# Kernel tuning notes

Hardware: AMD Instinct MI355X
Metric: run time of the kernel (lower is better)

## Reference

```python
import jax, jax.numpy as jnp
import numpy as np

N_NODES = 50000
N_EDGES = 400000
IN_DIM = 64
HID = 128
HEADS = 4
NEG_SLOPE = 0.2


def gat_conv(x, src, dst, W, a_src, a_dst, b, heads, out_ch, concat):
    N = x.shape[0]
    h = (x @ W).reshape(N, heads, out_ch)                 # [N,H,C]
    alpha_s = jnp.einsum('nhc,hc->nh', h, a_src)          # [N,H]
    alpha_d = jnp.einsum('nhc,hc->nh', h, a_dst)
    e = jax.nn.leaky_relu(alpha_s[src] + alpha_d[dst], NEG_SLOPE)  # [E,H]
    m = jax.ops.segment_max(e, dst, num_segments=N)
    m = jnp.where(jnp.isfinite(m), m, 0.0)
    ex = jnp.exp(e - m[dst])
    s = jax.ops.segment_sum(ex, dst, num_segments=N)
    alpha = ex / s[dst]                                   # segment softmax over incoming edges
    out = jax.ops.segment_sum(h[src] * alpha[:, :, None], dst, num_segments=N)  # [N,H,C]
    out = out.reshape(N, heads * out_ch) if concat else out.mean(axis=1)
    return out + b


def setup_inputs() -> dict:
    key = jax.random.key(0)
    ks = jax.random.split(key, 20)
    g = lambda i, shape, sc: (jax.random.normal(ks[i], shape, jnp.float32) * sc)
    x = g(0, (N_NODES, IN_DIM), 1.0)
    edge_index = jax.random.randint(ks[1], (2, N_EDGES), 0, N_NODES, dtype=jnp.int32)
    d = {
        'x': x, 'edge_index': edge_index,
        'W1': g(2, (IN_DIM, HEADS * HID), 0.1), 'a_src1': g(3, (HEADS, HID), 0.1), 'a_dst1': g(4, (HEADS, HID), 0.1), 'b1': jnp.zeros((HEADS * HID,), jnp.float32),
        'W2': g(5, (HEADS * HID, HEADS * HID), 0.05), 'a_src2': g(6, (HEADS, HID), 0.1), 'a_dst2': g(7, (HEADS, HID), 0.1), 'b2': jnp.zeros((HEADS * HID,), jnp.float32),
        'W3': g(8, (HEADS * HID, HID), 0.05), 'a_src3': g(9, (1, HID), 0.1), 'a_dst3': g(10, (1, HID), 0.1), 'b3': jnp.zeros((HID,), jnp.float32),
        'fc1_w': g(11, (HID, HID // 2), 0.1), 'fc1_b': jnp.zeros((HID // 2,), jnp.float32),
        'fc2_w': g(12, (HID // 2, 1), 0.1), 'fc2_b': jnp.zeros((1,), jnp.float32),
    }
    return d


def reference(x, edge_index, W1, a_src1, a_dst1, b1, W2, a_src2, a_dst2, b2, W3, a_src3, a_dst3, b3, fc1_w, fc1_b, fc2_w, fc2_b):
    N = x.shape[0]
    loop = jnp.arange(N, dtype=edge_index.dtype)
    src = jnp.concatenate([edge_index[0], loop])  # PyG GATConv adds self-loops by default
    dst = jnp.concatenate([edge_index[1], loop])
    h = jax.nn.elu(gat_conv(x, src, dst, W1, a_src1, a_dst1, b1, HEADS, HID, True))
    h = jax.nn.elu(gat_conv(h, src, dst, W2, a_src2, a_dst2, b2, HEADS, HID, True))
    h = jax.nn.elu(gat_conv(h, src, dst, W3, a_src3, a_dst3, b3, 1, HID, False))
    h = jax.nn.relu(h @ fc1_w + fc1_b)
    return jax.nn.sigmoid(h @ fc2_w + fc2_b)  # [N, 1]
```

## Files before the change

### kernel.cpp

```cpp
#include <hip/hip_runtime.h>
#include <math.h>

typedef __attribute__((ext_vector_type(8))) short short8;
typedef __attribute__((ext_vector_type(4))) float f32x4;
typedef unsigned short u16;
typedef unsigned int u32;

__device__ inline u16 f2b(float f) {
  u32 u = __float_as_uint(f);
  return (u16)((u + 0x7FFFu + ((u >> 16) & 1u)) >> 16);
}
__device__ inline float b2f(u16 b) { return __uint_as_float((u32)b << 16); }
__device__ inline float lrelu(float v) { return v > 0.f ? v : 0.2f * v; }

__device__ inline void gld_lds16(const void* g, void* l) {
  __builtin_amdgcn_global_load_lds((const __attribute__((address_space(1))) void*)g,
                                   (__attribute__((address_space(3))) void*)l, 16, 0, 0);
}

__global__ void cast_f32_bf16(const float* __restrict__ src, u16* __restrict__ dst, int n) {
  int i = blockIdx.x * blockDim.x + threadIdx.x;
  if (i < n) dst[i] = f2b(src[i]);
}

__global__ void cast_transpose_w(const float* __restrict__ W, u16* __restrict__ Wt, int K,
                                 int HC) {
  int i = blockIdx.x * blockDim.x + threadIdx.x;
  if (i >= K * HC) return;
  int k = i / HC, n = i % HC;
  Wt[(size_t)n * K + k] = f2b(W[i]);
}

__global__ __launch_bounds__(256) void gemm_bf16_gat(
    const u16* __restrict__ A, const u16* __restrict__ Bt, u16* __restrict__ Hb,
    const float* __restrict__ a_src, const float* __restrict__ a_dst,
    float* __restrict__ aS, float* __restrict__ aD, int M, int HC, int K, int Hh) {
  __shared__ u16 As[128 * 32];
  __shared__ u16 Bs[128 * 32];
  __shared__ float sRed[2][2][128];
  const int tid = threadIdx.x;
  const int w = tid >> 6, lane = tid & 63;
  const int wm = w >> 1, wn = w & 1;
  const int q = lane >> 4, l15 = lane & 15;
  const int nBase = blockIdx.x * 128;
  const int mBase = blockIdx.y * 128;
  const int h = nBase >> 7;
  const int srow = lane >> 2;
  const int skc = (lane & 3) * 8;

  f32x4 acc[4][4];
#pragma unroll
  for (int i = 0; i < 4; ++i)
#pragma unroll
    for (int j = 0; j < 4; ++j) acc[i][j] = (f32x4){0.f, 0.f, 0.f, 0.f};

  for (int k0 = 0; k0 < K; k0 += 32) {
#pragma unroll
    for (int r = 0; r < 2; ++r) {
      int lrow = w * 32 + r * 16 + srow;
      int ga = mBase + lrow;
      if (ga >= M) ga = M - 1;
      gld_lds16(A + (size_t)ga * K + k0 + skc, &As[(w * 32 + r * 16) * 32]);
      int gb = nBase + lrow;
      gld_lds16(Bt + (size_t)gb * K + k0 + skc, &Bs[(w * 32 + r * 16) * 32]);
    }
    __syncthreads();
    short8 af[4], bf[4];
#pragma unroll
    for (int i = 0; i < 4; ++i)
      af[i] = *(const short8*)&As[(wm * 64 + i * 16 + l15) * 32 + q * 8];
#pragma unroll
    for (int j = 0; j < 4; ++j)
      bf[j] = *(const short8*)&Bs[(wn * 64 + j * 16 + l15) * 32 + q * 8];
#pragma unroll
    for (int i = 0; i < 4; ++i)
#pragma unroll
      for (int j = 0; j < 4; ++j)
        acc[i][j] = __builtin_amdgcn_mfma_f32_16x16x32_bf16(af[i], bf[j], acc[i][j], 0, 0, 0);
    __syncthreads();
  }

  float asv[4], adv[4];
#pragma unroll
  for (int j = 0; j < 4; ++j) {
    int cw = wn * 64 + j * 16 + l15;
    asv[j] = a_src[h * 128 + cw];
    adv[j] = a_dst[h * 128 + cw];
  }
#pragma unroll
  for (int mi = 0; mi < 4; ++mi) {
#pragma unroll
    for (int r = 0; r < 4; ++r) {
      int row = mBase + wm * 64 + mi * 16 + q * 4 + r;
      float s = 0.f, d = 0.f;
#pragma unroll
      for (int j = 0; j < 4; ++j) {
        float v = acc[mi][j][r];
        s = fmaf(v, asv[j], s);
        d = fmaf(v, adv[j], d);
        if (row < M) Hb[(size_t)row * HC + nBase + wn * 64 + j * 16 + l15] = f2b(v);
      }
#pragma unroll
      for (int o = 8; o; o >>= 1) {
        s += __shfl_xor(s, o);
        d += __shfl_xor(d, o);
      }
      if (l15 == 0) {
        int lr = wm * 64 + mi * 16 + q * 4 + r;
        sRed[0][wn][lr] = s;
        sRed[1][wn][lr] = d;
      }
    }
  }
  __syncthreads();
  if (tid < 128) {
    int row = mBase + tid;
    if (row < M) {
      aS[(size_t)row * Hh + h] = sRed[0][0][tid] + sRed[0][1][tid];
      aD[(size_t)row * Hh + h] = sRed[1][0][tid] + sRed[1][1][tid];
    }
  }
}

__device__ inline void edge_nodes(const int* __restrict__ ei, int E0, int e, int& s, int& d) {
  if (e < E0) { s = ei[e]; d = ei[E0 + e]; }
  else        { s = e - E0; d = e - E0; }
}

__global__ void deg_count(const int* __restrict__ ei, int E0, int ET, int* __restrict__ deg) {
  int e = blockIdx.x * blockDim.x + threadIdx.x;
  if (e >= ET) return;
  int s, d;
  edge_nodes(ei, E0, e, s, d);
  atomicAdd(&deg[d], 1);
}

__global__ __launch_bounds__(256) void scan_chunk(const int* __restrict__ deg,
                                                  int* __restrict__ incl,
                                                  int* __restrict__ bsums, int N) {
  __shared__ int sdata[256];
  const int t = threadIdx.x;
  const int base = blockIdx.x * 2048;
  int v[8];
  int sum = 0;
#pragma unroll
  for (int i = 0; i < 8; ++i) {
    int idx = base + t * 8 + i;
    v[i] = (idx < N) ? deg[idx] : 0;
    sum += v[i];
  }
  sdata[t] = sum;
  __syncthreads();
  for (int off = 1; off < 256; off <<= 1) {
    int x = (t >= off) ? sdata[t - off] : 0;
    __syncthreads();
    sdata[t] += x;
    __syncthreads();
  }
  int run = (t > 0) ? sdata[t - 1] : 0;
#pragma unroll
  for (int i = 0; i < 8; ++i) {
    int idx = base + t * 8 + i;
    run += v[i];
    if (idx < N) incl[idx] = run;
  }
  if (t == 255) bsums[blockIdx.x] = sdata[255];
}

__global__ __launch_bounds__(256) void scan_bsums(int* __restrict__ bsums, int nb) {
  __shared__ int s[256];
  int t = threadIdx.x;
  s[t] = (t < nb) ? bsums[t] : 0;
  __syncthreads();
  for (int off = 1; off < 256; off <<= 1) {
    int x = (t >= off) ? s[t - off] : 0;
    __syncthreads();
    s[t] += x;
    __syncthreads();
  }
  if (t < nb) bsums[t] = (t == 0) ? 0 : s[t - 1];
}

__global__ void scan_final(const int* __restrict__ incl, const int* __restrict__ bsums,
                           int* __restrict__ rowptr, int N) {
  int i = blockIdx.x * blockDim.x + threadIdx.x;
  if (i < N) rowptr[i + 1] = incl[i] + bsums[i >> 11];
  if (i == 0) rowptr[0] = 0;
}

__global__ void csr_fill(const int* __restrict__ ei, int E0, int ET,
                         const int* __restrict__ rowptr, int* __restrict__ cnt,
                         int* __restrict__ csr_src) {
  int e = blockIdx.x * blockDim.x + threadIdx.x;
  if (e >= ET) return;
  int s, d;
  edge_nodes(ei, E0, e, s, d);
  int pos = atomicAdd(&cnt[d], 1);
  csr_src[rowptr[d] + pos] = s;
}

__global__ __launch_bounds__(256) void gat_fused_agg(
    const int* __restrict__ rowptr, const int* __restrict__ csr_src,
    const u16* __restrict__ Hb, const float* __restrict__ aSb,
    const float* __restrict__ aDb, const float* __restrict__ bias,
    u16* __restrict__ outB, float* __restrict__ outF, int N, int Hh) {
  const int wid = (int)((blockIdx.x * (blockDim.x >> 6)) + (threadIdx.x >> 6));
  const int lane = threadIdx.x & 63;
  if (wid >= N) return;
  const int beg = rowptr[wid];
  const int deg = rowptr[wid + 1] - beg;

  if (Hh == 4) {
    const int h = lane >> 4;
    const int e16 = lane & 15;
    const int c0 = lane * 8;
    const float adh = aDb[(size_t)wid * 4 + h];
    float bv[8];
    *(float4*)&bv[0] = *(const float4*)&bias[c0];
    *(float4*)&bv[4] = *(const float4*)&bias[c0 + 4];
    float m = -1e30f, ssum = 0.f;
    float acc[8] = {};
    for (int c = 0; c < deg; c += 16) {
      const int ce = min(16, deg - c);
      int srcv = 0;
      float l = -1e30f;
      if (e16 < ce) {
        srcv = csr_src[beg + c + e16];
        l = lrelu(aSb[(size_t)srcv * 4 + h] + adh);
      }
      float cm = l;
#pragma unroll
      for (int o = 8; o; o >>= 1) cm = fmaxf(cm, __shfl_xor(cm, o));
      float newm = fmaxf(m, cm);
      float r = expf(m - newm);
      m = newm;
      float pexp = expf(l - m);
      float cs = pexp;
#pragma unroll
      for (int o = 8; o; o >>= 1) cs += __shfl_xor(cs, o);
      ssum = ssum * r + cs;
#pragma unroll
      for (int i = 0; i < 8; ++i) acc[i] *= r;
      const int hbase = lane & 48;
      for (int e = 0; e < ce; ++e) {
        int se = __shfl(srcv, e);
        float wgt = __shfl(pexp, hbase | e);
        uint4 pv = *(const uint4*)&Hb[(size_t)se * 512 + c0];
        acc[0] = fmaf(wgt, b2f((u16)(pv.x & 0xffff)), acc[0]);
        acc[1] = fmaf(wgt, b2f((u16)(pv.x >> 16)), acc[1]);
        acc[2] = fmaf(wgt, b2f((u16)(pv.y & 0xffff)), acc[2]);
        acc[3] = fmaf(wgt, b2f((u16)(pv.y >> 16)), acc[3]);
        acc[4] = fmaf(wgt, b2f((u16)(pv.z & 0xffff)), acc[4]);
        acc[5] = fmaf(wgt, b2f((u16)(pv.z >> 16)), acc[5]);
        acc[6] = fmaf(wgt, b2f((u16)(pv.w & 0xffff)), acc[6]);
        acc[7] = fmaf(wgt, b2f((u16)(pv.w >> 16)), acc[7]);
      }
    }
    const float inv = 1.f / ssum;
    u16 packed[8];
#pragma unroll
    for (int i = 0; i < 8; ++i) {
      float v = fmaf(acc[i], inv, bv[i]);
      v = v > 0.f ? v : expm1f(v);
      acc[i] = v;
      packed[i] = f2b(v);
    }
    if (outB) *(uint4*)&outB[(size_t)wid * 512 + c0] = *(const uint4*)packed;
    if (outF) {
      *(float4*)&outF[(size_t)wid * 512 + c0] = make_float4(acc[0], acc[1], acc[2], acc[3]);
      *(float4*)&outF[(size_t)wid * 512 + c0 + 4] =
          make_float4(acc[4], acc[5], acc[6], acc[7]);
    }
  } else {
    const int c0 = lane * 2;
    const float adh = aDb[wid];
    const float bv0 = bias[c0], bv1 = bias[c0 + 1];
    float m = -1e30f, ssum = 0.f;
    float a0 = 0.f, a1 = 0.f;
    for (int c = 0; c < deg; c += 64) {
      const int ce = min(64, deg - c);
      int srcv = 0;
      float l = -1e30f;
      if (lane < ce) {
        srcv = csr_src[beg + c + lane];
        l = lrelu(aSb[srcv] + adh);
      }
      float cm = l;
#pragma unroll
      for (int o = 32; o; o >>= 1) cm = fmaxf(cm, __shfl_xor(cm, o));
      float newm = fmaxf(m, cm);
      float r = expf(m - newm);
      m = newm;
      float pexp = expf(l - m);
      float cs = pexp;
#pragma unroll
      for (int o = 32; o; o >>= 1) cs += __shfl_xor(cs, o);
      ssum = ssum * r + cs;
      a0 *= r;
      a1 *= r;
      for (int e = 0; e < ce; ++e) {
        int se = __shfl(srcv, e);
        float wgt = __shfl(pexp, e);
        u32 pv = *(const u32*)&Hb[(size_t)se * 128 + c0];
        a0 = fmaf(wgt, b2f((u16)(pv & 0xffff)), a0);
        a1 = fmaf(wgt, b2f((u16)(pv >> 16)), a1);
      }
    }
    const float inv = 1.f / ssum;
    float v0 = fmaf(a0, inv, bv0), v1 = fmaf(a1, inv, bv1);
    v0 = v0 > 0.f ? v0 : expm1f(v0);
    v1 = v1 > 0.f ? v1 : expm1f(v1);
    if (outB) {
      u16 pk[2] = {f2b(v0), f2b(v1)};
      *(u32*)&outB[(size_t)wid * 128 + c0] = *(const u32*)pk;
    }
    if (outF) *(float2*)&outF[(size_t)wid * 128 + c0] = make_float2(v0, v1);
  }
}

__global__ __launch_bounds__(256) void fc_head(const float* __restrict__ A,
                                               const float* __restrict__ B,
                                               const float* __restrict__ bias,
                                               const float* __restrict__ w2,
                                               const float* __restrict__ b2,
                                               float* __restrict__ out, int M) {
  __shared__ float As[16][64];
  __shared__ float Bs[16][64];
  __shared__ float sP[64][17];
  const int tid = threadIdx.x;
  const int tx = tid & 15, ty = tid >> 4;
  const int mBase = blockIdx.y * 64;
  const int aRow = tid >> 2;
  const int aK = (tid & 3) << 2;
  const int bC = tid & 63;
  const int bR0 = tid >> 6;
  const int K = 128, N = 64;
  float acc[4][4] = {};
  for (int k0 = 0; k0 < K; k0 += 16) {
    float4 av = make_float4(0.f, 0.f, 0.f, 0.f);
    int gr = mBase + aRow;
    if (gr < M) av = *(const float4*)&A[(size_t)gr * K + k0 + aK];
    As[aK + 0][aRow] = av.x;
    As[aK + 1][aRow] = av.y;
    As[aK + 2][aRow] = av.z;
    As[aK + 3][aRow] = av.w;
#pragma unroll
    for (int i = 0; i < 4; ++i) {
      int r = bR0 + i * 4;
      Bs[r][bC] = B[(size_t)(k0 + r) * N + bC];
    }
    __syncthreads();
#pragma unroll
    for (int k = 0; k < 16; ++k) {
      float4 a = *(const float4*)&As[k][ty * 4];
      float4 b = *(const float4*)&Bs[k][tx * 4];
      float ar[4] = {a.x, a.y, a.z, a.w};
      float br[4] = {b.x, b.y, b.z, b.w};
#pragma unroll
      for (int i = 0; i < 4; ++i)
#pragma unroll
        for (int j = 0; j < 4; ++j) acc[i][j] = fmaf(ar[i], br[j], acc[i][j]);
    }
    __syncthreads();
  }
  float4 bv = *(const float4*)&bias[tx * 4];
  float4 wv = *(const float4*)&w2[tx * 4];
#pragma unroll
  for (int i = 0; i < 4; ++i) {
    float p = 0.f;
    p = fmaf(fmaxf(acc[i][0] + bv.x, 0.f), wv.x, p);
    p = fmaf(fmaxf(acc[i][1] + bv.y, 0.f), wv.y, p);
    p = fmaf(fmaxf(acc[i][2] + bv.z, 0.f), wv.z, p);
    p = fmaf(fmaxf(acc[i][3] + bv.w, 0.f), wv.w, p);
    sP[ty * 4 + i][tx] = p;
  }
  __syncthreads();
  if (tid < 64) {
    int row = mBase + tid;
    if (row < M) {
      float s = 0.f;
#pragma unroll
      for (int t = 0; t < 16; ++t) s += sP[tid][t];
      out[row] = 1.f / (1.f + expf(-(s + b2[0])));
    }
  }
}

extern "C" void kernel_launch(void* const* d_in, const int* in_sizes, int n_in,
                              void* d_out, int out_size, void* d_ws, size_t ws_size,
                              hipStream_t stream) {
  const float* x    = (const float*)d_in[0];
  const int*   ei   = (const int*)d_in[1];
  const float* W1   = (const float*)d_in[2];
  const float* as1  = (const float*)d_in[3];
  const float* ad1  = (const float*)d_in[4];
  const float* b1   = (const float*)d_in[5];
  const float* W2   = (const float*)d_in[6];
  const float* as2  = (const float*)d_in[7];
  const float* ad2  = (const float*)d_in[8];
  const float* b2   = (const float*)d_in[9];
  const float* W3   = (const float*)d_in[10];
  const float* as3  = (const float*)d_in[11];
  const float* ad3  = (const float*)d_in[12];
  const float* b3   = (const float*)d_in[13];
  const float* fc1w = (const float*)d_in[14];
  const float* fc1b = (const float*)d_in[15];
  const float* fc2w = (const float*)d_in[16];
  const float* fc2b = (const float*)d_in[17];
  float* out = (float*)d_out;

  const int N  = in_sizes[0] / 64;
  const int E0 = in_sizes[1] / 2;
  const int ET = E0 + N;

  char* ws = (char*)d_ws;
  size_t off = 0;
  auto alloc = [&](size_t bytes) -> void* {
    void* p = ws + off;
    off += (bytes + 255) & ~(size_t)255;
    return p;
  };
  u16*   bufXb   = (u16*)alloc((size_t)N * 512 * 2);
  u16*   bufHb   = (u16*)alloc((size_t)N * 512 * 2);
  float* bufF    = (float*)alloc((size_t)N * 128 * 4);
  float* aS      = (float*)alloc((size_t)N * 4 * 4);
  float* aD      = (float*)alloc((size_t)N * 4 * 4);
  u16*   Wt1     = (u16*)alloc((size_t)512 * 64 * 2);
  u16*   Wt2     = (u16*)alloc((size_t)512 * 512 * 2);
  u16*   Wt3     = (u16*)alloc((size_t)128 * 512 * 2);
  int*   deg     = (int*)alloc((size_t)N * 4);
  int*   cnt     = (int*)alloc((size_t)N * 4);
  int*   incl    = (int*)alloc((size_t)N * 4);
  int*   rowptr  = (int*)alloc((size_t)(N + 1) * 4);
  int*   bsums   = (int*)alloc(256 * 4);
  int*   csr_src = (int*)alloc((size_t)ET * 4);
  (void)ws_size; (void)n_in; (void)out_size;

  hipLaunchKernelGGL(cast_f32_bf16, dim3((N * 64 + 255) / 256), dim3(256), 0, stream, x,
                     bufXb, N * 64);
  hipLaunchKernelGGL(cast_transpose_w, dim3((64 * 512 + 255) / 256), dim3(256), 0, stream,
                     W1, Wt1, 64, 512);
  hipLaunchKernelGGL(cast_transpose_w, dim3((512 * 512 + 255) / 256), dim3(256), 0, stream,
                     W2, Wt2, 512, 512);
  hipLaunchKernelGGL(cast_transpose_w, dim3((512 * 128 + 255) / 256), dim3(256), 0, stream,
                     W3, Wt3, 512, 128);

  hipMemsetAsync(deg, 0, (size_t)N * 4, stream);
  hipMemsetAsync(cnt, 0, (size_t)N * 4, stream);
  int eb = (ET + 255) / 256;
  hipLaunchKernelGGL(deg_count, dim3(eb), dim3(256), 0, stream, ei, E0, ET, deg);
  int nb = (N + 2047) / 2048;
  hipLaunchKernelGGL(scan_chunk, dim3(nb), dim3(256), 0, stream, deg, incl, bsums, N);
  hipLaunchKernelGGL(scan_bsums, dim3(1), dim3(256), 0, stream, bsums, nb);
  hipLaunchKernelGGL(scan_final, dim3((N + 255) / 256), dim3(256), 0, stream, incl, bsums,
                     rowptr, N);
  hipLaunchKernelGGL(csr_fill, dim3(eb), dim3(256), 0, stream, ei, E0, ET, rowptr, cnt,
                     csr_src);

  const int gy = (N + 127) / 128;
  auto gat_layer = [&](int K, const u16* Wt, const float* a_s, const float* a_d,
                       const float* bias, int Hh, u16* aggB, float* aggF) {
    const int HC = Hh * 128;
    hipLaunchKernelGGL(gemm_bf16_gat, dim3(HC / 128, gy), dim3(256), 0, stream, bufXb, Wt,
                       bufHb, a_s, a_d, aS, aD, N, HC, K, Hh);
    hipLaunchKernelGGL(gat_fused_agg, dim3((N + 3) / 4), dim3(256), 0, stream, rowptr,
                       csr_src, bufHb, aS, aD, bias, aggB, aggF, N, Hh);
  };

  gat_layer(64,  Wt1, as1, ad1, b1, 4, bufXb, nullptr);
  gat_layer(512, Wt2, as2, ad2, b2, 4, bufXb, nullptr);
  gat_layer(512, Wt3, as3, ad3, b3, 1, nullptr, bufF);

  hipLaunchKernelGGL(fc_head, dim3(1, (N + 63) / 64), dim3(256), 0, stream, bufF, fc1w,
                     fc1b, fc2w, fc2b, out, N);
}
```

Before: 475.2 us.

## Fuse prep kernels, drop bsums scan, unroll aggregation gather by four

Merges the x cast, three weight cast-transposes and degree counting into one fused_prep launch, and merges the two memsets into one. The separate bsums scan kernel is removed; scan_final now sums the preceding chunk totals serially per thread. The aggregation loops peel the first chunk to skip the rescale and unroll the edge gather by four so more independent loads are in flight. Together these cut launch overhead and raise memory-level parallelism, at the cost of a branchier prep kernel and redundant bsums reads in scan_final.

```diff
diff --git a/kernel.cpp b/kernel.cpp
--- a/kernel.cpp
+++ b/kernel.cpp
@@ -18,17 +18,40 @@
                                    (__attribute__((address_space(3))) void*)l, 16, 0, 0);
 }
 
-__global__ void cast_f32_bf16(const float* __restrict__ src, u16* __restrict__ dst, int n) {
+__global__ void fused_prep(const float* __restrict__ x, u16* __restrict__ xb, int NX,
+                           const float* __restrict__ W1, u16* __restrict__ Wt1,
+                           const float* __restrict__ W2, u16* __restrict__ Wt2,
+                           const float* __restrict__ W3, u16* __restrict__ Wt3,
+                           const int* __restrict__ ei, int E0, int ET,
+                           int* __restrict__ deg) {
   int i = blockIdx.x * blockDim.x + threadIdx.x;
-  if (i < n) dst[i] = f2b(src[i]);
-}
-
-__global__ void cast_transpose_w(const float* __restrict__ W, u16* __restrict__ Wt, int K,
-                                 int HC) {
-  int i = blockIdx.x * blockDim.x + threadIdx.x;
-  if (i >= K * HC) return;
-  int k = i / HC, n = i % HC;
-  Wt[(size_t)n * K + k] = f2b(W[i]);
+  if (i < NX) {
+    xb[i] = f2b(x[i]);
+    return;
+  }
+  i -= NX;
+  if (i < 64 * 512) {
+    int k = i / 512, n = i % 512;
+    Wt1[n * 64 + k] = f2b(W1[i]);
+    return;
+  }
+  i -= 64 * 512;
+  if (i < 512 * 512) {
+    int k = i / 512, n = i % 512;
+    Wt2[n * 512 + k] = f2b(W2[i]);
+    return;
+  }
+  i -= 512 * 512;
+  if (i < 512 * 128) {
+    int k = i / 128, n = i % 128;
+    Wt3[n * 512 + k] = f2b(W3[i]);
+    return;
+  }
+  i -= 512 * 128;
+  if (i < ET) {
+    int d = (i < E0) ? ei[E0 + i] : (i - E0);
+    atomicAdd(&deg[d], 1);
+  }
 }
 
 __global__ __launch_bounds__(256) void gemm_bf16_gat(
@@ -122,19 +145,6 @@
   }
 }
 
-__device__ inline void edge_nodes(const int* __restrict__ ei, int E0, int e, int& s, int& d) {
-  if (e < E0) { s = ei[e]; d = ei[E0 + e]; }
-  else        { s = e - E0; d = e - E0; }
-}
-
-__global__ void deg_count(const int* __restrict__ ei, int E0, int ET, int* __restrict__ deg) {
-  int e = blockIdx.x * blockDim.x + threadIdx.x;
-  if (e >= ET) return;
-  int s, d;
-  edge_nodes(ei, E0, e, s, d);
-  atomicAdd(&deg[d], 1);
-}
-
 __global__ __launch_bounds__(256) void scan_chunk(const int* __restrict__ deg,
                                                   int* __restrict__ incl,
                                                   int* __restrict__ bsums, int N) {
@@ -167,24 +177,14 @@
   if (t == 255) bsums[blockIdx.x] = sdata[255];
 }
 
-__global__ __launch_bounds__(256) void scan_bsums(int* __restrict__ bsums, int nb) {
-  __shared__ int s[256];
-  int t = threadIdx.x;
-  s[t] = (t < nb) ? bsums[t] : 0;
-  __syncthreads();
-  for (int off = 1; off < 256; off <<= 1) {
-    int x = (t >= off) ? s[t - off] : 0;
-    __syncthreads();
-    s[t] += x;
-    __syncthreads();
-  }
-  if (t < nb) bsums[t] = (t == 0) ? 0 : s[t - 1];
-}
-
 __global__ void scan_final(const int* __restrict__ incl, const int* __restrict__ bsums,
-                           int* __restrict__ rowptr, int N) {
+                           int* __restrict__ rowptr, int N, int nb) {
   int i = blockIdx.x * blockDim.x + threadIdx.x;
-  if (i < N) rowptr[i + 1] = incl[i] + bsums[i >> 11];
+  if (i >= N) return;
+  int chunk = i >> 11;
+  int pre = 0;
+  for (int j = 0; j < chunk; ++j) pre += bsums[j];
+  rowptr[i + 1] = incl[i] + pre;
   if (i == 0) rowptr[0] = 0;
 }
 
@@ -194,7 +194,8 @@
   int e = blockIdx.x * blockDim.x + threadIdx.x;
   if (e >= ET) return;
   int s, d;
-  edge_nodes(ei, E0, e, s, d);
+  if (e < E0) { s = ei[e]; d = ei[E0 + e]; }
+  else        { s = e - E0; d = e - E0; }
   int pos = atomicAdd(&cnt[d], 1);
   csr_src[rowptr[d] + pos] = s;
 }
@@ -214,6 +215,7 @@
     const int h = lane >> 4;
     const int e16 = lane & 15;
     const int c0 = lane * 8;
+    const int hbase = lane & 48;
     const float adh = aDb[(size_t)wid * 4 + h];
     float bv[8];
     *(float4*)&bv[0] = *(const float4*)&bias[c0];
@@ -231,29 +233,55 @@
       float cm = l;
 #pragma unroll
       for (int o = 8; o; o >>= 1) cm = fmaxf(cm, __shfl_xor(cm, o));
-      float newm = fmaxf(m, cm);
-      float r = expf(m - newm);
-      m = newm;
-      float pexp = expf(l - m);
-      float cs = pexp;
-#pragma unroll
-      for (int o = 8; o; o >>= 1) cs += __shfl_xor(cs, o);
-      ssum = ssum * r + cs;
-#pragma unroll
-      for (int i = 0; i < 8; ++i) acc[i] *= r;
-      const int hbase = lane & 48;
-      for (int e = 0; e < ce; ++e) {
+      float pexp, cs;
+      if (c == 0) {
+        m = cm;
+        pexp = expf(l - m);
+        cs = pexp;
+#pragma unroll
+        for (int o = 8; o; o >>= 1) cs += __shfl_xor(cs, o);
+        ssum = cs;
+      } else {
+        float newm = fmaxf(m, cm);
+        float r = expf(m - newm);
+        m = newm;
+        pexp = expf(l - m);
+        cs = pexp;
+#pragma unroll
+        for (int o = 8; o; o >>= 1) cs += __shfl_xor(cs, o);
+        ssum = ssum * r + cs;
+#pragma unroll
+        for (int i = 0; i < 8; ++i) acc[i] *= r;
+      }
+      int e = 0;
+      for (; e + 4 <= ce; e += 4) {
+        int se0 = __shfl(srcv, e + 0), se1 = __shfl(srcv, e + 1);
+        int se2 = __shfl(srcv, e + 2), se3 = __shfl(srcv, e + 3);
+        float w0 = __shfl(pexp, hbase | (e + 0)), w1 = __shfl(pexp, hbase | (e + 1));
+        float w2 = __shfl(pexp, hbase | (e + 2)), w3 = __shfl(pexp, hbase | (e + 3));
+        uint4 p0 = *(const uint4*)&Hb[(size_t)se0 * 512 + c0];
+        uint4 p1 = *(const uint4*)&Hb[(size_t)se1 * 512 + c0];
+        uint4 p2 = *(const uint4*)&Hb[(size_t)se2 * 512 + c0];
+        uint4 p3 = *(const uint4*)&Hb[(size_t)se3 * 512 + c0];
+#define ACC8(pv, wgt)                                             \
+  acc[0] = fmaf(wgt, b2f((u16)(pv.x & 0xffff)), acc[0]);          \
+  acc[1] = fmaf(wgt, b2f((u16)(pv.x >> 16)), acc[1]);             \
+  acc[2] = fmaf(wgt, b2f((u16)(pv.y & 0xffff)), acc[2]);          \
+  acc[3] = fmaf(wgt, b2f((u16)(pv.y >> 16)), acc[3]);             \
+  acc[4] = fmaf(wgt, b2f((u16)(pv.z & 0xffff)), acc[4]);          \
+  acc[5] = fmaf(wgt, b2f((u16)(pv.z >> 16)), acc[5]);             \
+  acc[6] = fmaf(wgt, b2f((u16)(pv.w & 0xffff)), acc[6]);          \
+  acc[7] = fmaf(wgt, b2f((u16)(pv.w >> 16)), acc[7]);
+        ACC8(p0, w0)
+        ACC8(p1, w1)
+        ACC8(p2, w2)
+        ACC8(p3, w3)
+      }
+      for (; e < ce; ++e) {
         int se = __shfl(srcv, e);
         float wgt = __shfl(pexp, hbase | e);
         uint4 pv = *(const uint4*)&Hb[(size_t)se * 512 + c0];
-        acc[0] = fmaf(wgt, b2f((u16)(pv.x & 0xffff)), acc[0]);
-        acc[1] = fmaf(wgt, b2f((u16)(pv.x >> 16)), acc[1]);
-        acc[2] = fmaf(wgt, b2f((u16)(pv.y & 0xffff)), acc[2]);
-        acc[3] = fmaf(wgt, b2f((u16)(pv.y >> 16)), acc[3]);
-        acc[4] = fmaf(wgt, b2f((u16)(pv.z & 0xffff)), acc[4]);
-        acc[5] = fmaf(wgt, b2f((u16)(pv.z >> 16)), acc[5]);
-        acc[6] = fmaf(wgt, b2f((u16)(pv.w & 0xffff)), acc[6]);
-        acc[7] = fmaf(wgt, b2f((u16)(pv.w >> 16)), acc[7]);
+        ACC8(pv, wgt)
       }
     }
     const float inv = 1.f / ssum;
@@ -288,17 +316,46 @@
       float cm = l;
 #pragma unroll
       for (int o = 32; o; o >>= 1) cm = fmaxf(cm, __shfl_xor(cm, o));
-      float newm = fmaxf(m, cm);
-      float r = expf(m - newm);
-      m = newm;
-      float pexp = expf(l - m);
-      float cs = pexp;
-#pragma unroll
-      for (int o = 32; o; o >>= 1) cs += __shfl_xor(cs, o);
-      ssum = ssum * r + cs;
-      a0 *= r;
-      a1 *= r;
-      for (int e = 0; e < ce; ++e) {
+      float pexp, cs;
+      if (c == 0) {
+        m = cm;
+        pexp = expf(l - m);
+        cs = pexp;
+#pragma unroll
+        for (int o = 32; o; o >>= 1) cs += __shfl_xor(cs, o);
+        ssum = cs;
+      } else {
+        float newm = fmaxf(m, cm);
+        float r = expf(m - newm);
+        m = newm;
+        pexp = expf(l - m);
+        cs = pexp;
+#pragma unroll
+        for (int o = 32; o; o >>= 1) cs += __shfl_xor(cs, o);
+        ssum = ssum * r + cs;
+        a0 *= r;
+        a1 *= r;
+      }
+      int e = 0;
+      for (; e + 4 <= ce; e += 4) {
+        int se0 = __shfl(srcv, e + 0), se1 = __shfl(srcv, e + 1);
+        int se2 = __shfl(srcv, e + 2), se3 = __shfl(srcv, e + 3);
+        float w0 = __shfl(pexp, e + 0), w1 = __shfl(pexp, e + 1);
+        float w2 = __shfl(pexp, e + 2), w3 = __shfl(pexp, e + 3);
+        u32 p0 = *(const u32*)&Hb[(size_t)se0 * 128 + c0];
+        u32 p1 = *(const u32*)&Hb[(size_t)se1 * 128 + c0];
+        u32 p2 = *(const u32*)&Hb[(size_t)se2 * 128 + c0];
+        u32 p3 = *(const u32*)&Hb[(size_t)se3 * 128 + c0];
+        a0 = fmaf(w0, b2f((u16)(p0 & 0xffff)), a0);
+        a1 = fmaf(w0, b2f((u16)(p0 >> 16)), a1);
+        a0 = fmaf(w1, b2f((u16)(p1 & 0xffff)), a0);
+        a1 = fmaf(w1, b2f((u16)(p1 >> 16)), a1);
+        a0 = fmaf(w2, b2f((u16)(p2 & 0xffff)), a0);
+        a1 = fmaf(w2, b2f((u16)(p2 >> 16)), a1);
+        a0 = fmaf(w3, b2f((u16)(p3 & 0xffff)), a0);
+        a1 = fmaf(w3, b2f((u16)(p3 >> 16)), a1);
+      }
+      for (; e < ce; ++e) {
         int se = __shfl(srcv, e);
         float wgt = __shfl(pexp, e);
         u32 pv = *(const u32*)&Hb[(size_t)se * 128 + c0];
@@ -428,32 +485,26 @@
   u16*   Wt1     = (u16*)alloc((size_t)512 * 64 * 2);
   u16*   Wt2     = (u16*)alloc((size_t)512 * 512 * 2);
   u16*   Wt3     = (u16*)alloc((size_t)128 * 512 * 2);
-  int*   deg     = (int*)alloc((size_t)N * 4);
-  int*   cnt     = (int*)alloc((size_t)N * 4);
+  int*   degcnt  = (int*)alloc((size_t)2 * N * 4);
+  int*   deg     = degcnt;
+  int*   cnt     = degcnt + N;
   int*   incl    = (int*)alloc((size_t)N * 4);
   int*   rowptr  = (int*)alloc((size_t)(N + 1) * 4);
   int*   bsums   = (int*)alloc(256 * 4);
   int*   csr_src = (int*)alloc((size_t)ET * 4);
   (void)ws_size; (void)n_in; (void)out_size;
 
-  hipLaunchKernelGGL(cast_f32_bf16, dim3((N * 64 + 255) / 256), dim3(256), 0, stream, x,
-                     bufXb, N * 64);
-  hipLaunchKernelGGL(cast_transpose_w, dim3((64 * 512 + 255) / 256), dim3(256), 0, stream,
-                     W1, Wt1, 64, 512);
-  hipLaunchKernelGGL(cast_transpose_w, dim3((512 * 512 + 255) / 256), dim3(256), 0, stream,
-                     W2, Wt2, 512, 512);
-  hipLaunchKernelGGL(cast_transpose_w, dim3((512 * 128 + 255) / 256), dim3(256), 0, stream,
-                     W3, Wt3, 512, 128);
-
-  hipMemsetAsync(deg, 0, (size_t)N * 4, stream);
-  hipMemsetAsync(cnt, 0, (size_t)N * 4, stream);
-  int eb = (ET + 255) / 256;
-  hipLaunchKernelGGL(deg_count, dim3(eb), dim3(256), 0, stream, ei, E0, ET, deg);
+  hipMemsetAsync(degcnt, 0, (size_t)2 * N * 4, stream);
+  const int NX = N * 64;
+  const int prepTotal = NX + 64 * 512 + 512 * 512 + 512 * 128 + ET;
+  hipLaunchKernelGGL(fused_prep, dim3((prepTotal + 255) / 256), dim3(256), 0, stream, x,
+                     bufXb, NX, W1, Wt1, W2, Wt2, W3, Wt3, ei, E0, ET, deg);
+
   int nb = (N + 2047) / 2048;
   hipLaunchKernelGGL(scan_chunk, dim3(nb), dim3(256), 0, stream, deg, incl, bsums, N);
-  hipLaunchKernelGGL(scan_bsums, dim3(1), dim3(256), 0, stream, bsums, nb);
   hipLaunchKernelGGL(scan_final, dim3((N + 255) / 256), dim3(256), 0, stream, incl, bsums,
-                     rowptr, N);
+                     rowptr, N, nb);
+  int eb = (ET + 255) / 256;
   hipLaunchKernelGGL(csr_fill, dim3(eb), dim3(256), 0, stream, ei, E0, ET, rowptr, cnt,
                      csr_src);
 
```

Result: faster. 463.4 us (-2.5%).
